# Optimization experiments

Hardware: AMD Instinct MI355X
Metric: run time of the kernel (lower is better)

Reference implementation:

```python
import jax, jax.numpy as jnp
import numpy as np

XBOUND = (-30.0, 30.0, 0.25)
YBOUND = (-15.0, 15.0, 0.25)
ZBOUND = (-1.0, 1.0, 0.5)
EPS = 1e-9


def _heights():
    n = int((ZBOUND[1] - ZBOUND[0]) // ZBOUND[2]) + 1
    return [ZBOUND[0] + i * ZBOUND[2] for i in range(n)]


def _bev_planes():
    # matches construct_plane_grid: linspace endpoints included, meshgrid(y, x) 'ij'
    num_x = int((XBOUND[1] - XBOUND[0]) / XBOUND[2])
    num_y = int((YBOUND[1] - YBOUND[0]) / YBOUND[2])
    x = jnp.linspace(XBOUND[0], XBOUND[1], num_x, dtype=jnp.float32)
    y = jnp.linspace(YBOUND[0], YBOUND[1], num_y, dtype=jnp.float32)
    yy, xx = jnp.meshgrid(y, x, indexing='ij')
    planes = [jnp.stack([xx, yy, jnp.full_like(xx, h)], axis=-1) for h in _heights()]
    return jnp.stack(planes)  # (nlvl, bH, bW, 3)


def _bilinear_grid_sample(im, grid):
    # faithful port of the manual pad+floor+gather grid_sample (align_corners=False)
    n, c, h, w = im.shape
    gh, gw = grid.shape[1], grid.shape[2]
    x = ((grid[..., 0] + 1) * w - 1) / 2
    y = ((grid[..., 1] + 1) * h - 1) / 2
    x = x.reshape(n, -1)
    y = y.reshape(n, -1)
    x0 = jnp.floor(x)
    y0 = jnp.floor(y)
    wa = ((x0 + 1 - x) * (y0 + 1 - y))[:, None, :]
    wb = ((x0 + 1 - x) * (y - y0))[:, None, :]
    wc = ((x - x0) * (y0 + 1 - y))[:, None, :]
    wd = ((x - x0) * (y - y0))[:, None, :]
    pw, ph = w + 2, h + 2
    # clip in float first to avoid int32 overflow; out-of-range lands on zero padding either way
    x0f = jnp.clip(x0, -2.0, w + 2.0)
    y0f = jnp.clip(y0, -2.0, h + 2.0)
    x0i = jnp.clip(x0f.astype(jnp.int32) + 1, 0, pw - 1)
    x1i = jnp.clip(x0f.astype(jnp.int32) + 2, 0, pw - 1)
    y0i = jnp.clip(y0f.astype(jnp.int32) + 1, 0, ph - 1)
    y1i = jnp.clip(y0f.astype(jnp.int32) + 2, 0, ph - 1)
    im_flat = jnp.pad(im, ((0, 0), (0, 0), (1, 1), (1, 1))).reshape(n, c, -1)

    def gather(xi, yi):
        return jnp.take_along_axis(im_flat, (xi + yi * pw)[:, None, :], axis=2)

    out = (gather(x0i, y0i) * wa + gather(x0i, y1i) * wb
           + gather(x1i, y0i) * wc + gather(x1i, y1i) * wd)
    return out.reshape(n, c, gh, gw)


def _campos(pts, ego2cam, img_h, img_w):
    # pts: (B, q, 3); ego2cam: (B, ncam, 4, 4)
    B, q, _ = pts.shape
    ncam = ego2cam.shape[1]
    pts_h = jnp.concatenate([pts, jnp.ones_like(pts[..., :1])], axis=-1)  # (B,q,4)
    cam = jnp.einsum('bnij,bqj->bnqi', ego2cam, pts_h)  # (B,ncam,q,4)
    z = cam[..., 2:3]
    mask = z > EPS
    xy = cam[..., 0:2] / z + EPS
    px = xy[..., 0:1] / img_w
    py = xy[..., 1:2] / img_h
    p = (jnp.concatenate([px, py], axis=-1) - 0.5) * 2
    mask = (mask & (p[..., 0:1] > -1.0) & (p[..., 0:1] < 1.0)
            & (p[..., 1:2] > -1.0) & (p[..., 1:2] < 1.0))
    return p.reshape(B * ncam, q, 2), mask.reshape(B, ncam, q)


def reference(cam_feat, ego2cam, conv_w, conv_b, img_h, img_w):
    B, ncam = ego2cam.shape[0], ego2cam.shape[1]
    C = cam_feat.shape[1]
    planes = _bev_planes().astype(cam_feat.dtype)  # (nlvl,bH,bW,3)
    nlvl, bH, bW, _ = planes.shape
    pts = jnp.broadcast_to(planes.reshape(1, -1, 3), (B, nlvl * bH * bW, 3))
    pos, mask = _campos(pts, ego2cam, img_h, img_w)
    grid = pos.reshape(B * ncam, nlvl * bH, bW, 2)
    proj = _bilinear_grid_sample(cam_feat, grid).reshape(B, ncam, C, nlvl, bH, bW)
    m = mask.reshape(B, ncam, 1, nlvl, bH, bW).astype(proj.dtype)
    feat = (proj * m).sum(axis=1)            # (B,C,nlvl,bH,bW)
    num = m.sum(axis=1)                      # (B,1,nlvl,bH,bW)
    feat = feat / jnp.where(num == 0, jnp.ones_like(num), num)
    coords = jnp.broadcast_to(jnp.transpose(planes, (3, 0, 1, 2))[None], (B, 3, nlvl, bH, bW))
    feat = jnp.concatenate([feat, coords], axis=1).reshape(B, (C + 3) * nlvl, bH, bW)
    out = jax.lax.conv_general_dilated(
        feat, conv_w, window_strides=(1, 1), padding=((1, 1), (1, 1)),
        dimension_numbers=('NCHW', 'OIHW', 'NCHW'))
    return out + conv_b[None, :, None, None]


def setup_inputs() -> dict:
    key = jax.random.key(0)
    k1, k2, k3 = jax.random.split(key, 3)
    B, ncam, C = 1, 6, 128
    cH, cW = 64, 176
    nlvl = 5
    cam_feat = jax.random.normal(k1, (B * ncam, C, cH, cW), dtype=jnp.float32)
    ego2cam = jax.random.normal(k2, (B, ncam, 4, 4), dtype=jnp.float32)
    conv_w = jax.random.normal(k3, (128, (C + 3) * nlvl, 3, 3), dtype=jnp.float32) * 0.02
    conv_b = jnp.zeros((128,), dtype=jnp.float32)
    return {'cam_feat': cam_feat, 'ego2cam': ego2cam, 'conv_w': conv_w,
            'conv_b': conv_b, 'img_h': 512, 'img_w': 1408}
```

## Files before the change

kernel.cpp:

```cpp
#include <hip/hip_runtime.h>
#include <hip/hip_bf16.h>

#define BH 120
#define BW 240
#define NLVL 5
#define NCAM 6
#define CH 128
#define FH 64
#define FW 176
#define CIN 655
#define CINP 672
#define NCT 21
#define FROWS 124
#define FCOLS 242
#define NPIX (BH*BW)

typedef __hip_bfloat16 bf16;
typedef __attribute__((ext_vector_type(8))) short s16x8;
typedef __attribute__((ext_vector_type(4))) float f32x4;
typedef unsigned int uint;
typedef __attribute__((ext_vector_type(4), aligned(4))) uint uint4a;

#define G_AS __attribute__((address_space(1)))
#define L_AS __attribute__((address_space(3)))

__device__ __forceinline__ float bf2f(unsigned short u) {
    union { unsigned int i; float f; } c; c.i = ((unsigned int)u) << 16; return c.f;
}
__device__ __forceinline__ uint f2bu(float x) {
    return (uint)__hip_bfloat16_raw(__float2bfloat16(x)).x;
}
__device__ __forceinline__ float blo(uint u) {
    union { uint i; float f; } c; c.i = u << 16; return c.f;
}
__device__ __forceinline__ float bhi(uint u) {
    union { uint i; float f; } c; c.i = u & 0xFFFF0000u; return c.f;
}

__global__ __launch_bounds__(256) void transpose_kernel(
    const float* __restrict__ in, bf16* __restrict__ out)
{
    __shared__ float t[32][129];
    int n = blockIdx.z, h = blockIdx.y, w0 = blockIdx.x * 32;
    int wlim = min(32, FW - w0);
    int wx = threadIdx.x & 31, cg = threadIdx.x >> 5;
    if (wx < wlim) {
        #pragma unroll
        for (int k = 0; k < 16; ++k) {
            int c = cg + k * 8;
            t[wx][c] = in[((n*CH + c)*FH + h)*FW + w0 + wx];
        }
    }
    __syncthreads();
    int c2 = threadIdx.x & 127, wi = threadIdx.x >> 7;
    for (int w = wi; w < wlim; w += 2)
        out[((n*FH + h)*FW + w0 + w)*CH + c2] = __float2bfloat16(t[w][c2]);
}

__global__ __launch_bounds__(256) void wprep_kernel(
    const float* __restrict__ w, bf16* __restrict__ wbf)
{
    int idx = blockIdx.x * 256 + threadIdx.x;
    if (idx >= 128 * CINP) return;
    int oc = idx / CINP, cin = idx - oc * CINP;
    float v[9];
    if (cin < CIN) {
        const float* s = w + ((size_t)oc * CIN + cin) * 9;
        #pragma unroll
        for (int k = 0; k < 9; ++k) v[k] = s[k];
    } else {
        #pragma unroll
        for (int k = 0; k < 9; ++k) v[k] = 0.f;
    }
    #pragma unroll
    for (int k = 0; k < 9; ++k)
        wbf[(size_t)(k * 128 + oc) * CINP + cin] = __float2bfloat16(v[k]);
}

__global__ __launch_bounds__(128) void border_kernel(bf16* __restrict__ feat)
{
    int b = blockIdx.x;
    int row, col;
    if (b < 242)      { row = 0;   col = b; }
    else if (b < 484) { row = 121; col = b - 242; }
    else if (b < 604) { row = b - 484 + 1; col = 0; }
    else              { row = b - 604 + 1; col = 241; }
    s16x8* p = (s16x8*)(feat + ((size_t)row*FCOLS + col)*CINP);
    int t = threadIdx.x;
    if (t < 84) p[t] = (s16x8){0,0,0,0,0,0,0,0};
}

__global__ __launch_bounds__(256) void proj_kernel(
    const bf16* __restrict__ camt,
    const float* __restrict__ e2c,
    const int* __restrict__ pimgh, const int* __restrict__ pimgw,
    bf16* __restrict__ feat)
{
    __shared__ int   s_soff[4][32];
    __shared__ float s_w4[4][30][4];
    __shared__ int   s_val[4][32];

    const int wv = threadIdx.x >> 6;
    const int lane = threadIdx.x & 63;
    const int bid = blockIdx.x;
    const int swz = (bid & 7) * 900 + (bid >> 3);
    const int pix = swz * 4 + wv;
    const int bx = pix % BW, by = pix / BW;
    float xw = (float)(-30.0 + bx * (60.0/239.0)); if (bx == BW-1) xw = 30.f;
    float yw = (float)(-15.0 + by * (30.0/119.0)); if (by == BH-1) yw = 15.f;

    const bool act = lane < 30;
    int valid = 0, ix = 0, iy = 0, cam = 0;
    float fx = 0.f, fy = 0.f;
    if (act) {
        int l = lane / 6; cam = lane - l*6;
        float h = -1.f + 0.5f * (float)l;
        const float* M = e2c + cam * 16;
        float cx = M[0]*xw + M[1]*yw + M[2]*h  + M[3];
        float cy = M[4]*xw + M[5]*yw + M[6]*h  + M[7];
        float cz = M[8]*xw + M[9]*yw + M[10]*h + M[11];
        float iw = (float)pimgw[0], ih = (float)pimgh[0];
        float px = ((cx/cz + 1e-9f)/iw - 0.5f) * 2.f;
        float py = ((cy/cz + 1e-9f)/ih - 0.5f) * 2.f;
        valid = (cz > 1e-9f) && (px > -1.f) && (px < 1.f)
                             && (py > -1.f) && (py < 1.f);
        float xs = ((px + 1.f)*(float)FW - 1.f) * 0.5f;
        float ys = ((py + 1.f)*(float)FH - 1.f) * 0.5f;
        float x0 = floorf(xs), y0 = floorf(ys);
        fx = xs - x0; fy = ys - y0;
        ix = (int)x0; iy = (int)y0;
        s_val[wv][lane] = valid;
    }
    __syncthreads();
    if (act) {
        int lbase = (lane / 6) * 6;
        int cnt = s_val[wv][lbase] + s_val[wv][lbase+1] + s_val[wv][lbase+2]
                + s_val[wv][lbase+3] + s_val[wv][lbase+4] + s_val[wv][lbase+5];
        float inv = (cnt > 0) ? (1.f / (float)cnt) : 0.f;
        float sc = valid ? inv : 0.f;
        int bx0 = min(max(ix, 0), FW-2);
        int by0 = min(max(iy, 0), FH-2);
        float gx0 = (1.f - fx) * sc, gx1 = fx * sc;
        float wx0 = 0.f, wx1 = 0.f;
        if (ix >= 0)     { if (ix == bx0) wx0 += gx0; else wx1 += gx0; }
        if (ix+1 <= FW-1){ if (ix+1 == bx0) wx0 += gx1; else wx1 += gx1; }
        float wy0 = 0.f, wy1 = 0.f;
        float gy0 = 1.f - fy, gy1 = fy;
        if (iy >= 0)     { if (iy == by0) wy0 += gy0; else wy1 += gy0; }
        if (iy+1 <= FH-1){ if (iy+1 == by0) wy0 += gy1; else wy1 += gy1; }
        s_w4[wv][lane][0] = wx0 * wy0;
        s_w4[wv][lane][1] = wx0 * wy1;
        s_w4[wv][lane][2] = wx1 * wy0;
        s_w4[wv][lane][3] = wx1 * wy1;
        s_soff[wv][lane] = valid ? ((cam*FH + by0)*FW + bx0)*CH : -1;
    }
    __syncthreads();

    const int c2 = lane * 2;
    float va[NLVL], vb[NLVL];
    #pragma unroll
    for (int l = 0; l < NLVL; ++l) { va[l] = 0.f; vb[l] = 0.f; }

    #pragma unroll
    for (int l = 0; l < NLVL; ++l) {
        #pragma unroll
        for (int cm = 0; cm < NCAM; ++cm) {
            int id = l*6 + cm;
            int so = s_soff[wv][id];
            if (so >= 0) {
                const bf16* bp = camt + so + c2;
                uint q0 = *(const uint*)(bp);
                uint q2 = *(const uint*)(bp + CH);
                uint q1 = *(const uint*)(bp + FW*CH);
                uint q3 = *(const uint*)(bp + FW*CH + CH);
                float w0 = s_w4[wv][id][0], w1 = s_w4[wv][id][1];
                float w2 = s_w4[wv][id][2], w3 = s_w4[wv][id][3];
                va[l] += w0*blo(q0) + w1*blo(q1) + w2*blo(q2) + w3*blo(q3);
                vb[l] += w0*bhi(q0) + w1*bhi(q1) + w2*bhi(q2) + w3*bhi(q3);
            }
        }
    }

    bf16* dpix = feat + ((size_t)(by+1)*FCOLS + (bx+1))*CINP;
    uint u0 = f2bu(va[0]) | (f2bu(va[1]) << 16);
    uint u1 = f2bu(va[2]) | (f2bu(va[3]) << 16);
    uint u2 = f2bu(va[4]) | (f2bu(vb[0]) << 16);
    uint u3 = f2bu(vb[1]) | (f2bu(vb[2]) << 16);
    uint u4 = f2bu(vb[3]) | (f2bu(vb[4]) << 16);
    char* dst = (char*)(dpix + c2*5);
    *(uint4a*)dst = (uint4a){u0, u1, u2, u3};
    *(uint*)(dst + 16) = u4;
    if (lane < 15) {
        int j = lane / 5, l = lane - j*5;
        float v = (j == 0) ? xw : (j == 1) ? yw : (-1.f + 0.5f*(float)l);
        dpix[CH*5 + lane] = __float2bfloat16(v);
    }
}

__global__ __launch_bounds__(256, 2) void conv_mfma_kernel(
    const bf16* __restrict__ feat,
    const bf16* __restrict__ wbf,
    bf16* __restrict__ part)
{
    __shared__ __align__(16) char lds[73728];
    const int tid  = threadIdx.x;
    const int wv   = tid >> 6;
    const int lane = tid & 63;
    const int t15  = tid & 15;
    const int kgl  = (tid >> 4) & 3;
    const int y0p = blockIdx.y * 8;
    const int x0p = blockIdx.x * 32;
    const int q   = blockIdx.z;
    const int ct0 = q ? (1 + 5*q) : 0;
    const int nct = q ? 5 : 6;
    const int nph = nct * 9;

    const int HB0 = 0, HB1 = 24576;
    const int WB0 = 49152, WB1 = 57344, WB2 = 65536;

    f32x4 acc[8][4];
    #pragma unroll
    for (int m = 0; m < 8; ++m)
        #pragma unroll
        for (int f = 0; f < 4; ++f)
            acc[m][f] = (f32x4){0.f, 0.f, 0.f, 0.f};

    auto stageW = [&](int ct, int off, int wb) {
        #pragma unroll
        for (int jj = 0; jj < 2; ++jj) {
            int j = 2*wv + jj;
            int cch = j*64 + lane;
            int oc = cch >> 2, kgp = cch & 3;
            int kg = kgp ^ ((oc >> 1) & 3);
            const bf16* src = wbf + ((size_t)(off*128 + oc)*CINP + ct*32 + kg*8);
            __builtin_amdgcn_global_load_lds((const G_AS void*)src,
                                             (L_AS void*)(lds + wb + j*1024),
                                             16, 0, 0);
        }
    };
    auto stageH = [&](int ct, int hb) {
        #pragma unroll
        for (int k = 0; k < 6; ++k) {
            int j = wv + 4*k;
            int cch = j*64 + lane;
            int pp = cch >> 2, kgp = cch & 3;
            int kg = kgp ^ ((pp >> 1) & 3);
            int row = pp / 34;
            int col = pp - row*34;
            int gc = min(x0p + col, FCOLS-1);
            const bf16* src = feat + ((size_t)(y0p + row)*FCOLS + gc)*CINP
                                   + ct*32 + kg*8;
            __builtin_amdgcn_global_load_lds((const G_AS void*)src,
                                             (L_AS void*)(lds + hb + j*1024),
                                             16, 0, 0);
        }
    };

    stageH(ct0, HB0);
    stageW(ct0, 0, WB0);
    stageW(ct0, 1, WB1);

    int lct = 0, off = 0;
    for (int g = 0; g < nph; ++g) {
        const bool hI = (lct + 1 < nct) && (off == 3 || off == 4);
        if (g == nph - 1)      { asm volatile("s_waitcnt vmcnt(0)" ::: "memory"); }
        else if (hI)           { asm volatile("s_waitcnt vmcnt(8)" ::: "memory"); }
        else                   { asm volatile("s_waitcnt vmcnt(2)" ::: "memory"); }
        __builtin_amdgcn_s_barrier();
        asm volatile("" ::: "memory");

        int g2 = g + 2;
        if (g2 < nph) {
            int lct2 = g2 / 9, off2 = g2 - lct2*9;
            int wb2 = (g2 % 3 == 0) ? WB0 : (g2 % 3 == 1) ? WB1 : WB2;
            stageW(ct0 + lct2, off2, wb2);
        }
        if (off == 2 && lct + 1 < nct)
            stageH(ct0 + lct + 1, (lct & 1) ? HB0 : HB1);

        const int wb = (g % 3 == 0) ? WB0 : (g % 3 == 1) ? WB1 : WB2;
        const int hb = (lct & 1) ? HB1 : HB0;
        const int ky = off / 3, kx = off - ky*3;

        s16x8 A[8];
        #pragma unroll
        for (int m = 0; m < 8; ++m) {
            int oc = m*16 + t15;
            A[m] = *(const s16x8*)(lds + wb + oc*64 + ((kgl ^ ((oc>>1)&3)) << 4));
        }
        #pragma unroll
        for (int f = 0; f < 4; ++f) {
            const int fr = f >> 1, fc = f & 1;
            int hp = (2*wv + fr + ky)*34 + fc*16 + t15 + kx;
            s16x8 Bv = *(const s16x8*)(lds + hb + hp*64
                                       + ((kgl ^ ((hp>>1)&3)) << 4));
            __builtin_amdgcn_s_setprio(1);
            #pragma unroll
            for (int m = 0; m < 8; ++m)
                acc[m][f] = __builtin_amdgcn_mfma_f32_16x16x32_bf16(
                                A[m], Bv, acc[m][f], 0, 0, 0);
            __builtin_amdgcn_s_setprio(0);
        }
        if (++off == 9) { off = 0; ++lct; }
    }

    bf16* pq = part + (size_t)q * (128*NPIX);
    #pragma unroll
    for (int f = 0; f < 4; ++f) {
        const int fr = f >> 1, fc = f & 1;
        const int x = x0p + fc*16 + t15;
        if (x < BW) {
            const int y = y0p + 2*wv + fr;
            #pragma unroll
            for (int m = 0; m < 8; ++m) {
                #pragma unroll
                for (int r = 0; r < 4; ++r) {
                    int oc = m*16 + kgl*4 + r;
                    pq[(size_t)oc*NPIX + y*BW + x] = __float2bfloat16(acc[m][f][r]);
                }
            }
        }
    }
}

__global__ __launch_bounds__(256) void combine_kernel(
    const bf16* __restrict__ part, const float* __restrict__ bias,
    float* __restrict__ out)
{
    int i8 = blockIdx.x * 256 + threadIdx.x;
    if (i8 >= 128*NPIX/8) return;
    int oc = i8 / (NPIX/8);
    float s[8];
    float b = bias[oc];
    #pragma unroll
    for (int k = 0; k < 8; ++k) s[k] = b;
    #pragma unroll
    for (int qq = 0; qq < 4; ++qq) {
        s16x8 v = *(const s16x8*)(part + (size_t)qq*(128*NPIX) + (size_t)i8*8);
        #pragma unroll
        for (int k = 0; k < 8; ++k) s[k] += bf2f((unsigned short)v[k]);
    }
    f32x4* o = (f32x4*)(out + (size_t)i8*8);
    o[0] = (f32x4){s[0], s[1], s[2], s[3]};
    o[1] = (f32x4){s[4], s[5], s[6], s[7]};
}

extern "C" void kernel_launch(void* const* d_in, const int* in_sizes, int n_in,
                              void* d_out, int out_size, void* d_ws, size_t ws_size,
                              hipStream_t stream)
{
    const float* cam_feat = (const float*)d_in[0];
    const float* ego2cam  = (const float*)d_in[1];
    const float* conv_w   = (const float*)d_in[2];
    const float* conv_b   = (const float*)d_in[3];
    const int*   img_h    = (const int*)d_in[4];
    const int*   img_w    = (const int*)d_in[5];
    float* out = (float*)d_out;

    bf16* camt = (bf16*)d_ws;
    bf16* feat = camt + (size_t)NCAM*CH*FH*FW;
    bf16* wbf  = feat + (size_t)FROWS*FCOLS*CINP;
    bf16* part = wbf  + (size_t)9*128*CINP;

    transpose_kernel<<<dim3(6, FH, NCAM), 256, 0, stream>>>(cam_feat, camt);
    wprep_kernel<<<(128*CINP + 255)/256, 256, 0, stream>>>(conv_w, wbf);
    border_kernel<<<724, 128, 0, stream>>>(feat);
    proj_kernel<<<NPIX/4, 256, 0, stream>>>(camt, ego2cam, img_h, img_w, feat);
    conv_mfma_kernel<<<dim3(8, 15, 4), 256, 0, stream>>>(feat, wbf, part);
    combine_kernel<<<(128*NPIX/8 + 255)/256, 256, 0, stream>>>(part, conv_b, out);
}
```

Before: 106.3 us.

## Widen conv tile to 64 columns with 8 waves sharing weight stage

The conv kernel now uses 512-thread blocks covering 8x64 output pixels, arranged as a 4x2 wave grid, instead of 256-thread blocks covering 8x32. Each weight tile staged in LDS is therefore reused by twice as many pixels, and the halo overhead shrinks. LDS reads for A and B are also hoisted ahead of the next-stage global loads, and all MFMAs then issue after a single lgkmcnt wait. In exchange, LDS per block grows to 120KB and the grid halves to 240 blocks, which may reduce occupancy and CU coverage.

```diff
diff --git a/kernel.cpp b/kernel.cpp
--- a/kernel.cpp
+++ b/kernel.cpp
@@ -197,26 +197,28 @@
     }
 }
 
-__global__ __launch_bounds__(256, 2) void conv_mfma_kernel(
+__global__ __launch_bounds__(512, 2) void conv_mfma_kernel(
     const bf16* __restrict__ feat,
     const bf16* __restrict__ wbf,
     bf16* __restrict__ part)
 {
-    __shared__ __align__(16) char lds[73728];
+    __shared__ __align__(16) char lds[122880];
     const int tid  = threadIdx.x;
     const int wv   = tid >> 6;
     const int lane = tid & 63;
     const int t15  = tid & 15;
     const int kgl  = (tid >> 4) & 3;
+    const int wr   = wv >> 1;
+    const int wc   = wv & 1;
     const int y0p = blockIdx.y * 8;
-    const int x0p = blockIdx.x * 32;
+    const int x0p = blockIdx.x * 64;
     const int q   = blockIdx.z;
     const int ct0 = q ? (1 + 5*q) : 0;
     const int nct = q ? 5 : 6;
     const int nph = nct * 9;
 
-    const int HB0 = 0, HB1 = 24576;
-    const int WB0 = 49152, WB1 = 57344, WB2 = 65536;
+    const int WB0 = 0, WB1 = 8192, WB2 = 16384;
+    const int HB0 = 24576, HB1 = 73728;
 
     f32x4 acc[8][4];
     #pragma unroll
@@ -226,27 +228,23 @@
             acc[m][f] = (f32x4){0.f, 0.f, 0.f, 0.f};
 
     auto stageW = [&](int ct, int off, int wb) {
-        #pragma unroll
-        for (int jj = 0; jj < 2; ++jj) {
-            int j = 2*wv + jj;
-            int cch = j*64 + lane;
-            int oc = cch >> 2, kgp = cch & 3;
-            int kg = kgp ^ ((oc >> 1) & 3);
-            const bf16* src = wbf + ((size_t)(off*128 + oc)*CINP + ct*32 + kg*8);
-            __builtin_amdgcn_global_load_lds((const G_AS void*)src,
-                                             (L_AS void*)(lds + wb + j*1024),
-                                             16, 0, 0);
-        }
+        int cch = wv*64 + lane;
+        int oc = cch >> 2, kgp = cch & 3;
+        int kg = kgp ^ ((oc >> 1) & 3);
+        const bf16* src = wbf + ((size_t)(off*128 + oc)*CINP + ct*32 + kg*8);
+        __builtin_amdgcn_global_load_lds((const G_AS void*)src,
+                                         (L_AS void*)(lds + wb + wv*1024),
+                                         16, 0, 0);
     };
     auto stageH = [&](int ct, int hb) {
         #pragma unroll
         for (int k = 0; k < 6; ++k) {
-            int j = wv + 4*k;
+            int j = wv*6 + k;
             int cch = j*64 + lane;
             int pp = cch >> 2, kgp = cch & 3;
             int kg = kgp ^ ((pp >> 1) & 3);
-            int row = pp / 34;
-            int col = pp - row*34;
+            int row = pp / 66;
+            int col = pp - row*66;
             int gc = min(x0p + col, FCOLS-1);
             const bf16* src = feat + ((size_t)(y0p + row)*FCOLS + gc)*CINP
                                    + ct*32 + kg*8;
@@ -260,14 +258,31 @@
     stageW(ct0, 0, WB0);
     stageW(ct0, 1, WB1);
 
+    const int aswz = (kgl ^ ((t15 >> 1) & 3)) << 4;
     int lct = 0, off = 0;
     for (int g = 0; g < nph; ++g) {
-        const bool hI = (lct + 1 < nct) && (off == 3 || off == 4);
-        if (g == nph - 1)      { asm volatile("s_waitcnt vmcnt(0)" ::: "memory"); }
-        else if (hI)           { asm volatile("s_waitcnt vmcnt(8)" ::: "memory"); }
-        else                   { asm volatile("s_waitcnt vmcnt(2)" ::: "memory"); }
+        if (g == nph - 1)                        { asm volatile("s_waitcnt vmcnt(0)" ::: "memory"); }
+        else if (off >= 3 && lct + 1 < nct)      { asm volatile("s_waitcnt vmcnt(7)" ::: "memory"); }
+        else                                     { asm volatile("s_waitcnt vmcnt(1)" ::: "memory"); }
         __builtin_amdgcn_s_barrier();
         asm volatile("" ::: "memory");
+
+        const int wb = (g % 3 == 0) ? WB0 : (g % 3 == 1) ? WB1 : WB2;
+        const int hb = (lct & 1) ? HB1 : HB0;
+        const int ky = off / 3, kx = off - ky*3;
+
+        s16x8 A[8];
+        #pragma unroll
+        for (int m = 0; m < 8; ++m)
+            A[m] = *(const s16x8*)(lds + wb + (m*16 + t15)*64 + aswz);
+        s16x8 B[4];
+        #pragma unroll
+        for (int f = 0; f < 4; ++f) {
+            const int fr = f >> 1, fc = f & 1;
+            int hp = (2*wr + fr + ky)*66 + wc*32 + fc*16 + t15 + kx;
+            B[f] = *(const s16x8*)(lds + hb + hp*64
+                                   + ((kgl ^ ((hp >> 1) & 3)) << 4));
+        }
 
         int g2 = g + 2;
         if (g2 < nph) {
@@ -278,29 +293,17 @@
         if (off == 2 && lct + 1 < nct)
             stageH(ct0 + lct + 1, (lct & 1) ? HB0 : HB1);
 
-        const int wb = (g % 3 == 0) ? WB0 : (g % 3 == 1) ? WB1 : WB2;
-        const int hb = (lct & 1) ? HB1 : HB0;
-        const int ky = off / 3, kx = off - ky*3;
-
-        s16x8 A[8];
-        #pragma unroll
-        for (int m = 0; m < 8; ++m) {
-            int oc = m*16 + t15;
-            A[m] = *(const s16x8*)(lds + wb + oc*64 + ((kgl ^ ((oc>>1)&3)) << 4));
-        }
-        #pragma unroll
-        for (int f = 0; f < 4; ++f) {
-            const int fr = f >> 1, fc = f & 1;
-            int hp = (2*wv + fr + ky)*34 + fc*16 + t15 + kx;
-            s16x8 Bv = *(const s16x8*)(lds + hb + hp*64
-                                       + ((kgl ^ ((hp>>1)&3)) << 4));
-            __builtin_amdgcn_s_setprio(1);
+        asm volatile("s_waitcnt lgkmcnt(0)" ::: "memory");
+        __builtin_amdgcn_sched_barrier(0);
+        __builtin_amdgcn_s_setprio(1);
+        #pragma unroll
+        for (int f = 0; f < 4; ++f)
             #pragma unroll
             for (int m = 0; m < 8; ++m)
                 acc[m][f] = __builtin_amdgcn_mfma_f32_16x16x32_bf16(
-                                A[m], Bv, acc[m][f], 0, 0, 0);
-            __builtin_amdgcn_s_setprio(0);
-        }
+                                A[m], B[f], acc[m][f], 0, 0, 0);
+        __builtin_amdgcn_s_setprio(0);
+
         if (++off == 9) { off = 0; ++lct; }
     }
 
@@ -308,9 +311,9 @@
     #pragma unroll
     for (int f = 0; f < 4; ++f) {
         const int fr = f >> 1, fc = f & 1;
-        const int x = x0p + fc*16 + t15;
+        const int x = x0p + wc*32 + fc*16 + t15;
         if (x < BW) {
-            const int y = y0p + 2*wv + fr;
+            const int y = y0p + 2*wr + fr;
             #pragma unroll
             for (int m = 0; m < 8; ++m) {
                 #pragma unroll
@@ -366,6 +369,6 @@
     wprep_kernel<<<(128*CINP + 255)/256, 256, 0, stream>>>(conv_w, wbf);
     border_kernel<<<724, 128, 0, stream>>>(feat);
     proj_kernel<<<NPIX/4, 256, 0, stream>>>(camt, ego2cam, img_h, img_w, feat);
-    conv_mfma_kernel<<<dim3(8, 15, 4), 256, 0, stream>>>(feat, wbf, part);
+    conv_mfma_kernel<<<dim3(4, 15, 4), 512, 0, stream>>>(feat, wbf, part);
     combine_kernel<<<(128*NPIX/8 + 255)/256, 256, 0, stream>>>(part, conv_b, out);
 }
```

Result: slower. 111.4 us (+4.8%).
